# Kernel tuning notes

Measured on AMD Instinct MI355X. Metric: run time of the kernel, lower is better.

The kernel has to match this reference:

```python
import jax, jax.numpy as jnp
import numpy as np

EPS = 1e-5
THRESHOLD = 0.2987


def conv3x3(x, w, stride=1):
    # x: [N,C,H,W], w: [O,I,3,3]
    return jax.lax.conv_general_dilated(
        x, w, window_strides=(stride, stride), padding=((1, 1), (1, 1)),
        dimension_numbers=("NCHW", "OIHW", "NCHW"))


def batchnorm_train(x, gamma, beta):
    # training-mode BN: batch statistics over (N,H,W), biased variance
    mean = jnp.mean(x, axis=(0, 2, 3), keepdims=True)
    var = jnp.var(x, axis=(0, 2, 3), keepdims=True)
    xhat = (x - mean) * jax.lax.rsqrt(var + EPS)
    return xhat * gamma[None, :, None, None] + beta[None, :, None, None]


def setup_inputs() -> dict:
    key = jax.random.key(0)
    k = jax.random.split(key, 7)
    N, C, H, W = 64, 128, 64, 64
    x = jax.random.normal(k[0], (N, C, H, W), dtype=jnp.float32)
    w1 = jax.random.normal(k[1], (C, C, 3, 3), dtype=jnp.float32) * (1.0 / np.sqrt(C * 9))
    gamma1 = jnp.ones((C,), dtype=jnp.float32)
    beta1 = jnp.zeros((C,), dtype=jnp.float32)
    w2 = jax.random.normal(k[2], (C, C, 3, 3), dtype=jnp.float32) * (1.0 / np.sqrt(C * 9))
    gamma2 = jnp.ones((C,), dtype=jnp.float32)
    beta2 = jnp.zeros((C,), dtype=jnp.float32)
    return {"x": x, "w1": w1, "gamma1": gamma1, "beta1": beta1,
            "w2": w2, "gamma2": gamma2, "beta2": beta2}


def reference(x, w1, gamma1, beta1, w2, gamma2, beta2):
    shortcut = x  # stride=1, no down_sample
    out = conv3x3(x, w1, stride=1)
    out = batchnorm_train(out, gamma1, beta1)
    out = jax.nn.relu(out)
    # per-(batch,channel) mean over H,W; zero channels whose mean < threshold
    channel_means = jnp.mean(out, axis=(2, 3))               # [N, C]
    mask = (channel_means >= THRESHOLD).astype(out.dtype)     # [N, C]
    out = out * mask[:, :, None, None]
    out = conv3x3(out, w2, stride=1)
    out = batchnorm_train(out, gamma2, beta2)
    out = out + shortcut
    out = jax.nn.relu(out)
    return out
```

## Files before the change

### kernel.cpp

```cpp
#include <hip/hip_runtime.h>

typedef short short8 __attribute__((ext_vector_type(8)));
typedef short short4v __attribute__((ext_vector_type(4)));
typedef float f32x4 __attribute__((ext_vector_type(4)));
typedef unsigned int u32;

#define EPSF 1e-5f
#define THRF 0.2987f

constexpr int N_ = 64, C_ = 128;
constexpr int PLANE = 4096;
constexpr size_t TENSOR = (size_t)N_ * C_ * PLANE;
constexpr int NHW = N_ * PLANE;
constexpr int PUNITS = 66 * 66 * 8;

__device__ __forceinline__ unsigned short f2bf(float f) {
    unsigned u = __float_as_uint(f);
    u += 0x7fffu + ((u >> 16) & 1u);
    return (unsigned short)(u >> 16);
}
__device__ __forceinline__ float bf2f(unsigned short h) {
    return __uint_as_float((unsigned)h << 16);
}
__device__ __forceinline__ void gld16(const unsigned short* g, unsigned short* l) {
    __builtin_amdgcn_global_load_lds(
        (const __attribute__((address_space(1))) u32*)g,
        (__attribute__((address_space(3))) u32*)l, 16, 0, 0);
}

__global__ __launch_bounds__(256) void prep_w_k(const float* __restrict__ w1,
                                                const float* __restrict__ w2,
                                                unsigned short* __restrict__ Wt1,
                                                unsigned short* __restrict__ Wt2) {
    int idx = blockIdx.x * 256 + threadIdx.x;
    const int sel = idx >= 147456;
    const float* src = sel ? w2 : w1;
    unsigned short* dst = sel ? Wt2 : Wt1;
    const int r = idx - sel * 147456;
    const int tap = r >> 14;
    const int rem = r & 16383;
    const int co = rem >> 7, ci = rem & 127;
    const int half = ci >> 6, csh = (ci >> 5) & 1;
    const int s = half * 18 + tap * 2 + csh;
    dst[(size_t)s * 4096 + co * 32 + (ci & 31)] = f2bf(src[(co * 128 + ci) * 9 + tap]);
}

__global__ __launch_bounds__(256) void zero_border_k(unsigned short* __restrict__ io) {
    int idx = blockIdx.x * 256 + threadIdx.x;
    if (idx >= 266240) return;
    const int plane = idx / 2080;
    const int t = idx - plane * 2080;
    int sp;
    if (t < 528) sp = t >> 3;
    else if (t < 1056) sp = 65 * 66 + ((t - 528) >> 3);
    else if (t < 1568) sp = (((t - 1056) >> 3) + 1) * 66;
    else sp = (((t - 1568) >> 3) + 1) * 66 + 65;
    const size_t off = ((size_t)plane * PUNITS + sp * 8 + (t & 7)) * 8;
    *(short8*)&io[off] = (short8){0, 0, 0, 0, 0, 0, 0, 0};
}

__global__ __launch_bounds__(256) void to_nhwc_k(const float* __restrict__ src,
                                                 unsigned short* __restrict__ dst) {
    __shared__ __align__(16) unsigned short tl[64 * 40];
    const int b = blockIdx.x;
    const int c0 = (b & 3) * 32;
    const int h  = (b >> 2) & 63;
    const int n  = b >> 8;
    const int t  = threadIdx.x;
    for (int i = t; i < 512; i += 256) {
        const int cl = i >> 4;
        const int c  = c0 + cl;
        const int w4 = (i & 15) * 4;
        float4 v = *(const float4*)&src[(size_t)(n * 128 + c) * 4096 + h * 64 + w4];
        tl[(w4 + 0) * 40 + cl] = f2bf(v.x);
        tl[(w4 + 1) * 40 + cl] = f2bf(v.y);
        tl[(w4 + 2) * 40 + cl] = f2bf(v.z);
        tl[(w4 + 3) * 40 + cl] = f2bf(v.w);
    }
    __syncthreads();
    const int w = t >> 2, cs = t & 3;
    short8 v = *(const short8*)&tl[w * 40 + cs * 8];
    const int c = c0 + cs * 8;
    const int half = c >> 6, cig = (c >> 3) & 7;
    const int colp = w + 1, rowp = h + 1;
    const size_t off = ((size_t)(half * 64 + n) * PUNITS
                        + (size_t)(rowp * 66 + colp) * 8 + (cig ^ (colp & 7))) * 8;
    *(short8*)&dst[off] = v;
}

template <int STAGE>
__global__ __launch_bounds__(256, 3) void conv_mfma_k(
    const unsigned short* __restrict__ inT, const unsigned short* __restrict__ Wt,
    const float* __restrict__ msA, const float* __restrict__ mhA,
    unsigned short* __restrict__ outB, float* __restrict__ part) {
    __shared__ __align__(16) unsigned short sIn[2112 * 8];
    __shared__ float fS[256], fQ[256];

    const int b  = (blockIdx.x & 7) * 256 + (blockIdx.x >> 3);
    const int h0 = (b & 31) * 2;
    const int n  = b >> 5;
    const int tid  = threadIdx.x;
    const int lane = tid & 63;
    const int wid  = tid >> 6;
    const int co_base = (wid >> 1) * 64;
    const int px_base = (wid & 1) * 64;
    const int lr = lane & 15;
    const int lg = lane >> 4;

    f32x4 acc[4][4];
#pragma unroll
    for (int i = 0; i < 4; ++i)
#pragma unroll
        for (int j = 0; j < 4; ++j) acc[i][j] = (f32x4){0.f, 0.f, 0.f, 0.f};

    const int nc = n * 128;
    const unsigned short* wlane = Wt + (size_t)(co_base + lr) * 32 + lg * 8;

    int ldsQ[4][2][3];
#pragma unroll
    for (int j = 0; j < 4; ++j) {
        const int px = px_base + j * 16 + lr;
        const int r = px >> 6, c = px & 63;
#pragma unroll
        for (int csh = 0; csh < 2; ++csh)
#pragma unroll
            for (int dc = 0; dc < 3; ++dc) {
                const int cig = csh * 4 + lg;
                ldsQ[j][csh][dc] = (r * 66 + c + dc) * 128 + (cig ^ ((c + dc) & 7)) * 16;
            }
    }

    auto stage_in = [&](int half) {
        const unsigned short* src =
            inT + ((size_t)(half * 64 + n) * PUNITS + (size_t)h0 * 66 * 8) * 8;
        if (STAGE == 1) {
            for (int c = wid; c < 33; c += 4)
                gld16(src + (c * 64 + lane) * 8, &sIn[c * 512]);
        } else {
            const int ncb = nc + half * 64;
            for (int i = tid; i < 2112; i += 256) {
                const int sp = i >> 3, ul = i & 7;
                const int rq = sp / 66;
                const int colp = sp - rq * 66;
                const int rp = h0 + rq;
                short8 v = {0, 0, 0, 0, 0, 0, 0, 0};
                if (rp != 0 && rp != 65 && colp != 0 && colp != 65) {
                    v = *(const short8*)&src[i * 8];
                    const int cig = ul ^ (colp & 7);
                    const int cb = ncb + cig * 8;
                    const float4 m0 = *(const float4*)&msA[cb];
                    const float4 m1 = *(const float4*)&msA[cb + 4];
                    const float4 a0 = *(const float4*)&mhA[cb];
                    const float4 a1 = *(const float4*)&mhA[cb + 4];
                    short8 w;
                    w[0] = (short)f2bf(fmaxf(fmaf(bf2f((unsigned short)v[0]), m0.x, a0.x), 0.f));
                    w[1] = (short)f2bf(fmaxf(fmaf(bf2f((unsigned short)v[1]), m0.y, a0.y), 0.f));
                    w[2] = (short)f2bf(fmaxf(fmaf(bf2f((unsigned short)v[2]), m0.z, a0.z), 0.f));
                    w[3] = (short)f2bf(fmaxf(fmaf(bf2f((unsigned short)v[3]), m0.w, a0.w), 0.f));
                    w[4] = (short)f2bf(fmaxf(fmaf(bf2f((unsigned short)v[4]), m1.x, a1.x), 0.f));
                    w[5] = (short)f2bf(fmaxf(fmaf(bf2f((unsigned short)v[5]), m1.y, a1.y), 0.f));
                    w[6] = (short)f2bf(fmaxf(fmaf(bf2f((unsigned short)v[6]), m1.z, a1.z), 0.f));
                    w[7] = (short)f2bf(fmaxf(fmaf(bf2f((unsigned short)v[7]), m1.w, a1.w), 0.f));
                    v = w;
                }
                *(short8*)&sIn[i * 8] = v;
            }
        }
    };

    auto ldw2 = [&](short8* dst, const unsigned short* p) {
#pragma unroll
        for (int i = 0; i < 4; ++i)
            dst[i] = *(const short8*)&p[i * 512];
    };
    auto ldb = [&](short8* bfv, int dr, int dc, int csh) {
#pragma unroll
        for (int j = 0; j < 4; ++j)
            bfv[j] = *(const short8*)((const char*)sIn + ldsQ[j][csh][dc] + dr * 8448);
    };
    auto mm = [&](short8* af, short8* bfv) {
        __builtin_amdgcn_s_setprio(1);
#pragma unroll
        for (int i = 0; i < 4; ++i)
#pragma unroll
            for (int j = 0; j < 4; ++j)
                acc[i][j] = __builtin_amdgcn_mfma_f32_16x16x32_bf16(af[i], bfv[j],
                                                                    acc[i][j], 0, 0, 0);
        __builtin_amdgcn_s_setprio(0);
    };

    short8 afA[4], afB[4], bfv[4];
    const unsigned short* wpA = wlane;
    const unsigned short* wpB = wlane + 4096;

    stage_in(0);
    ldw2(afA, wpA);
    ldw2(afB, wpB);
    __syncthreads();

#pragma unroll
    for (int half = 0; half < 2; ++half) {
#pragma unroll
        for (int it = 0; it < 9; ++it) {
            const int dr = it / 3, dc = it - dr * 3;
            ldb(bfv, dr, dc, 0);
            mm(afA, bfv);
            if (it < 8) { wpA += 8192; ldw2(afA, wpA); }
            ldb(bfv, dr, dc, 1);
            mm(afB, bfv);
            if (it < 8) { wpB += 8192; ldw2(afB, wpB); }
        }
        if (half == 0) {
            wpA += 8192; ldw2(afA, wpA);
            wpB += 8192; ldw2(afB, wpB);
            __syncthreads();
            stage_in(1);
            __syncthreads();
        }
    }

#pragma unroll
    for (int i = 0; i < 4; ++i)
#pragma unroll
        for (int q = 0; q < 4; ++q) {
            float v = acc[i][0][q] + acc[i][1][q] + acc[i][2][q] + acc[i][3][q];
            float w = acc[i][0][q] * acc[i][0][q] + acc[i][1][q] * acc[i][1][q]
                    + acc[i][2][q] * acc[i][2][q] + acc[i][3][q] * acc[i][3][q];
#pragma unroll
            for (int m = 1; m < 16; m <<= 1) {
                v += __shfl_xor(v, m);
                w += __shfl_xor(w, m);
            }
            if (lr == 0) {
                const int colocal = i * 16 + lg * 4 + q;
                fS[wid * 64 + colocal] = v;
                fQ[wid * 64 + colocal] = w;
            }
        }
    __syncthreads();
    if (tid < 128) {
        const int grp = tid >> 6, cl = tid & 63;
        part[(size_t)b * 256 + tid]       = fS[(grp * 2) * 64 + cl] + fS[(grp * 2 + 1) * 64 + cl];
        part[(size_t)b * 256 + 128 + tid] = fQ[(grp * 2) * 64 + cl] + fQ[(grp * 2 + 1) * 64 + cl];
    }

    if (STAGE == 1) {
        const int h = h0 + (px_base >> 6);
        const int rowp = h + 1;
        const size_t plane = (size_t)((co_base >> 6) * 64 + n) * PUNITS * 8;
        const int pg = lg >> 1;
#pragma unroll
        for (int j = 0; j < 4; ++j) {
            const int w = j * 16 + lr;
            const int colp = w + 1;
            const size_t spoff = plane + (size_t)(rowp * 66 + colp) * 8 * 8;
#pragma unroll
            for (int i = 0; i < 4; ++i) {
                u32 p0 = ((u32)f2bf(acc[i][j][1]) << 16) | f2bf(acc[i][j][0]);
                u32 p1 = ((u32)f2bf(acc[i][j][3]) << 16) | f2bf(acc[i][j][2]);
                const u32 q0 = __shfl_xor(p0, 16);
                const u32 q1 = __shfl_xor(p1, 16);
                if ((lg & 1) == 0) {
                    const int cig = (i * 2 + pg) & 7;
                    u32 st4[4] = {p0, p1, q0, q1};
                    *(short8*)&outB[spoff + (size_t)(cig ^ (colp & 7)) * 8] =
                        *(const short8*)st4;
                }
            }
        }
    } else {
        const size_t outN = (size_t)n * 128 * 4096;
#pragma unroll
        for (int i = 0; i < 4; ++i) {
            const int cob = co_base + i * 16 + lg * 4;
#pragma unroll
            for (int q = 0; q < 4; ++q) {
                unsigned short* op = outB + outN + (size_t)(cob + q) * 4096
                                     + h0 * 64 + px_base + lr;
#pragma unroll
                for (int j = 0; j < 4; ++j) op[j * 16] = f2bf(acc[i][j][q]);
            }
        }
    }
}

__global__ __launch_bounds__(256) void bn_finalize_k(const float* __restrict__ part,
                                                     const float* __restrict__ gamma,
                                                     const float* __restrict__ beta,
                                                     float* __restrict__ st) {
    const int c = blockIdx.x;
    float s = 0.f, q = 0.f;
    for (int b = threadIdx.x; b < 2048; b += 256) {
        s += part[(size_t)b * 256 + c];
        q += part[(size_t)b * 256 + 128 + c];
    }
    __shared__ float rs[256], rq[256];
    rs[threadIdx.x] = s; rq[threadIdx.x] = q;
    __syncthreads();
    for (int o = 128; o > 0; o >>= 1) {
        if (threadIdx.x < o) {
            rs[threadIdx.x] += rs[threadIdx.x + o];
            rq[threadIdx.x] += rq[threadIdx.x + o];
        }
        __syncthreads();
    }
    if (threadIdx.x == 0) {
        const float inv  = 1.f / (float)NHW;
        const float mean = rs[0] * inv;
        const float var  = rq[0] * inv - mean * mean;
        const float sc   = gamma[c] * rsqrtf(var + EPSF);
        st[c]       = sc;
        st[C_ + c]  = fmaf(-mean, sc, beta[c]);
    }
}

__global__ __launch_bounds__(256) void maskpart_k(const unsigned short* __restrict__ y1,
                                                  const float* __restrict__ st,
                                                  float* __restrict__ msA,
                                                  float* __restrict__ mhA) {
    const int n = blockIdx.x >> 1, half = blockIdx.x & 1;
    const int t = threadIdx.x;
    const int colg = t & 63;
    const int p = t >> 6;
    const int colp = 1 + colg;
    float scv[2][8], shv[2][8], a[2][8];
#pragma unroll
    for (int k = 0; k < 2; ++k)
#pragma unroll
        for (int e = 0; e < 8; ++e) {
            const int c = half * 64 + (2 * p + k) * 8 + e;
            scv[k][e] = st[c];
            shv[k][e] = st[128 + c];
            a[k][e] = 0.f;
        }
    const size_t plane = (size_t)(half * 64 + n) * PUNITS * 8;
    for (int rowp = 1; rowp <= 64; ++rowp) {
        const int sp = rowp * 66 + colp;
#pragma unroll
        for (int k = 0; k < 2; ++k) {
            const int cig = 2 * p + k;
            short8 v = *(const short8*)&y1[plane + ((size_t)sp * 8 + (cig ^ (colp & 7))) * 8];
#pragma unroll
            for (int e = 0; e < 8; ++e)
                a[k][e] += fmaxf(fmaf(bf2f((unsigned short)v[e]), scv[k][e], shv[k][e]), 0.f);
        }
    }
    __shared__ float lds[256][16];
#pragma unroll
    for (int k = 0; k < 2; ++k)
#pragma unroll
        for (int e = 0; e < 8; ++e) lds[t][k * 8 + e] = a[k][e];
    __syncthreads();
    if (t < 64) {
        const int cig = t >> 3, e = t & 7, p2 = cig >> 1, k2 = cig & 1;
        float s = 0.f;
        for (int cg = 0; cg < 64; ++cg) s += lds[p2 * 64 + cg][k2 * 8 + e];
        const int c = half * 64 + t;
        const float m = (s * (1.f / 4096.f) >= THRF) ? 1.f : 0.f;
        msA[n * 128 + c] = st[c] * m;
        mhA[n * 128 + c] = st[128 + c] * m;
    }
}

__global__ __launch_bounds__(256) void final_k(const unsigned short* __restrict__ y3,
                                               const float* __restrict__ x,
                                               const float* __restrict__ st,
                                               float* __restrict__ out) {
    const size_t total8 = TENSOR / 8;
    for (size_t g = (size_t)blockIdx.x * 256 + threadIdx.x; g < total8;
         g += (size_t)gridDim.x * 256) {
        const int c = (int)((g >> 9) & (C_ - 1));
        const float sc = st[c], sh = st[C_ + c];
        short8 yv = *(const short8*)&y3[g * 8];
        float4 a0 = ((const float4*)x)[g * 2];
        float4 a1 = ((const float4*)x)[g * 2 + 1];
        float4 o0, o1;
        o0.x = fmaxf(fmaf(bf2f((unsigned short)yv[0]), sc, sh) + a0.x, 0.f);
        o0.y = fmaxf(fmaf(bf2f((unsigned short)yv[1]), sc, sh) + a0.y, 0.f);
        o0.z = fmaxf(fmaf(bf2f((unsigned short)yv[2]), sc, sh) + a0.z, 0.f);
        o0.w = fmaxf(fmaf(bf2f((unsigned short)yv[3]), sc, sh) + a0.w, 0.f);
        o1.x = fmaxf(fmaf(bf2f((unsigned short)yv[4]), sc, sh) + a1.x, 0.f);
        o1.y = fmaxf(fmaf(bf2f((unsigned short)yv[5]), sc, sh) + a1.y, 0.f);
        o1.z = fmaxf(fmaf(bf2f((unsigned short)yv[6]), sc, sh) + a1.z, 0.f);
        o1.w = fmaxf(fmaf(bf2f((unsigned short)yv[7]), sc, sh) + a1.w, 0.f);
        ((float4*)out)[g * 2]     = o0;
        ((float4*)out)[g * 2 + 1] = o1;
    }
}

extern "C" void kernel_launch(void* const* d_in, const int* in_sizes, int n_in,
                              void* d_out, int out_size, void* d_ws, size_t ws_size,
                              hipStream_t stream) {
    const float* x  = (const float*)d_in[0];
    const float* w1 = (const float*)d_in[1];
    const float* g1 = (const float*)d_in[2];
    const float* b1 = (const float*)d_in[3];
    const float* w2 = (const float*)d_in[4];
    const float* g2 = (const float*)d_in[5];
    const float* b2 = (const float*)d_in[6];
    float* out = (float*)d_out;

    unsigned short* y1 = (unsigned short*)d_out;

    char* wsb = (char*)d_ws;
    unsigned short* io  = (unsigned short*)wsb;
    unsigned short* y3b = (unsigned short*)wsb;
    unsigned short* Wt1 = (unsigned short*)(wsb + (size_t)71368704);
    unsigned short* Wt2 = Wt1 + 147456;
    float* part = (float*)(wsb + (size_t)71368704 + 589824);
    float* st1  = part + 2048 * 256;
    float* st2  = st1 + 256;
    float* msA  = st2 + 256;
    float* mhA  = msA + 64 * 128;

    prep_w_k<<<1152, 256, 0, stream>>>(w1, w2, Wt1, Wt2);
    zero_border_k<<<1040, 256, 0, stream>>>(io);
    to_nhwc_k<<<16384, 256, 0, stream>>>(x, io);
    conv_mfma_k<1><<<2048, 256, 0, stream>>>(io, Wt1, nullptr, nullptr, y1, part);
    bn_finalize_k<<<128, 256, 0, stream>>>(part, g1, b1, st1);
    maskpart_k<<<128, 256, 0, stream>>>(y1, st1, msA, mhA);
    conv_mfma_k<2><<<2048, 256, 0, stream>>>(y1, Wt2, msA, mhA, y3b, part);
    bn_finalize_k<<<128, 256, 0, stream>>>(part, g2, b2, st2);
    final_k<<<8192, 256, 0, stream>>>(y3b, x, st2, out);
}
```

Baseline: 328.6 us.

## Prefetch second channel half into registers during MFMA loop; split mask reduction

```diff
diff --git a/kernel.cpp b/kernel.cpp
--- a/kernel.cpp
+++ b/kernel.cpp
@@ -130,14 +130,13 @@
             }
     }
 
-    auto stage_in = [&](int half) {
-        const unsigned short* src =
-            inT + ((size_t)(half * 64 + n) * PUNITS + (size_t)h0 * 66 * 8) * 8;
+    auto stage_h0 = [&]() {
+        const unsigned short* src = inT + ((size_t)n * PUNITS + (size_t)h0 * 66 * 8) * 8;
         if (STAGE == 1) {
             for (int c = wid; c < 33; c += 4)
                 gld16(src + (c * 64 + lane) * 8, &sIn[c * 512]);
         } else {
-            const int ncb = nc + half * 64;
+            const int ncb = nc;
             for (int i = tid; i < 2112; i += 256) {
                 const int sp = i >> 3, ul = i & 7;
                 const int rq = sp / 66;
@@ -189,14 +188,24 @@
         __builtin_amdgcn_s_setprio(0);
     };
 
-    short8 afA[4], afB[4], bfv[4];
+    short8 afA[4], afB[4], bfv[4], pre[9];
     const unsigned short* wpA = wlane;
     const unsigned short* wpB = wlane + 4096;
 
-    stage_in(0);
+    stage_h0();
     ldw2(afA, wpA);
     ldw2(afB, wpB);
     __syncthreads();
+
+    {
+        const unsigned short* src1 =
+            inT + ((size_t)(64 + n) * PUNITS + (size_t)h0 * 66 * 8) * 8;
+#pragma unroll
+        for (int k = 0; k < 8; ++k)
+            pre[k] = *(const short8*)&src1[(size_t)(tid + k * 256) * 8];
+        pre[8] = (tid < 64) ? *(const short8*)&src1[(size_t)(2048 + tid) * 8]
+                            : (short8){0, 0, 0, 0, 0, 0, 0, 0};
+    }
 
 #pragma unroll
     for (int half = 0; half < 2; ++half) {
@@ -214,7 +223,44 @@
             wpA += 8192; ldw2(afA, wpA);
             wpB += 8192; ldw2(afB, wpB);
             __syncthreads();
-            stage_in(1);
+            if (STAGE == 1) {
+#pragma unroll
+                for (int k = 0; k < 9; ++k) {
+                    const int idx = tid + k * 256;
+                    if (k < 8 || tid < 64)
+                        *(short8*)&sIn[(size_t)idx * 8] = pre[k];
+                }
+            } else {
+                const int ncb = nc + 64;
+#pragma unroll
+                for (int k = 0; k < 9; ++k) {
+                    const int idx = tid + k * 256;
+                    if (k == 8 && tid >= 64) continue;
+                    const int sp = idx >> 3, ul = idx & 7;
+                    const int rq = sp / 66;
+                    const int colp = sp - rq * 66;
+                    const int rp = h0 + rq;
+                    short8 v = {0, 0, 0, 0, 0, 0, 0, 0};
+                    if (rp != 0 && rp != 65 && colp != 0 && colp != 65) {
+                        const short8 pv = pre[k];
+                        const int cig = ul ^ (colp & 7);
+                        const int cb = ncb + cig * 8;
+                        const float4 m0 = *(const float4*)&msA[cb];
+                        const float4 m1 = *(const float4*)&msA[cb + 4];
+                        const float4 a0 = *(const float4*)&mhA[cb];
+                        const float4 a1 = *(const float4*)&mhA[cb + 4];
+                        v[0] = (short)f2bf(fmaxf(fmaf(bf2f((unsigned short)pv[0]), m0.x, a0.x), 0.f));
+                        v[1] = (short)f2bf(fmaxf(fmaf(bf2f((unsigned short)pv[1]), m0.y, a0.y), 0.f));
+                        v[2] = (short)f2bf(fmaxf(fmaf(bf2f((unsigned short)pv[2]), m0.z, a0.z), 0.f));
+                        v[3] = (short)f2bf(fmaxf(fmaf(bf2f((unsigned short)pv[3]), m0.w, a0.w), 0.f));
+                        v[4] = (short)f2bf(fmaxf(fmaf(bf2f((unsigned short)pv[4]), m1.x, a1.x), 0.f));
+                        v[5] = (short)f2bf(fmaxf(fmaf(bf2f((unsigned short)pv[5]), m1.y, a1.y), 0.f));
+                        v[6] = (short)f2bf(fmaxf(fmaf(bf2f((unsigned short)pv[6]), m1.z, a1.z), 0.f));
+                        v[7] = (short)f2bf(fmaxf(fmaf(bf2f((unsigned short)pv[7]), m1.w, a1.w), 0.f));
+                    }
+                    *(short8*)&sIn[(size_t)idx * 8] = v;
+                }
+            }
             __syncthreads();
         }
     }
@@ -316,9 +362,9 @@
 
 __global__ __launch_bounds__(256) void maskpart_k(const unsigned short* __restrict__ y1,
                                                   const float* __restrict__ st,
-                                                  float* __restrict__ msA,
-                                                  float* __restrict__ mhA) {
-    const int n = blockIdx.x >> 1, half = blockIdx.x & 1;
+                                                  float* __restrict__ qsum) {
+    const int blk = blockIdx.x;
+    const int n = blk >> 3, half = (blk >> 2) & 1, rq = blk & 3;
     const int t = threadIdx.x;
     const int colg = t & 63;
     const int p = t >> 6;
@@ -334,7 +380,7 @@
             a[k][e] = 0.f;
         }
     const size_t plane = (size_t)(half * 64 + n) * PUNITS * 8;
-    for (int rowp = 1; rowp <= 64; ++rowp) {
+    for (int rowp = rq * 16 + 1; rowp <= rq * 16 + 16; ++rowp) {
         const int sp = rowp * 66 + colp;
 #pragma unroll
         for (int k = 0; k < 2; ++k) {
@@ -355,11 +401,22 @@
         const int cig = t >> 3, e = t & 7, p2 = cig >> 1, k2 = cig & 1;
         float s = 0.f;
         for (int cg = 0; cg < 64; ++cg) s += lds[p2 * 64 + cg][k2 * 8 + e];
-        const int c = half * 64 + t;
-        const float m = (s * (1.f / 4096.f) >= THRF) ? 1.f : 0.f;
-        msA[n * 128 + c] = st[c] * m;
-        mhA[n * 128 + c] = st[128 + c] * m;
-    }
+        qsum[(size_t)blk * 64 + t] = s;
+    }
+}
+
+__global__ void maskfin_k(const float* __restrict__ qsum, const float* __restrict__ st,
+                          float* __restrict__ msA, float* __restrict__ mhA) {
+    const int n = blockIdx.x, c = threadIdx.x;
+    if (c >= 128) return;
+    const int half = c >> 6, cl = c & 63;
+    float s = 0.f;
+#pragma unroll
+    for (int rq = 0; rq < 4; ++rq)
+        s += qsum[(size_t)(n * 8 + half * 4 + rq) * 64 + cl];
+    const float m = (s * (1.f / 4096.f) >= THRF) ? 1.f : 0.f;
+    msA[n * 128 + c] = st[c] * m;
+    mhA[n * 128 + c] = st[128 + c] * m;
 }
 
 __global__ __launch_bounds__(256) void final_k(const unsigned short* __restrict__ y3,
@@ -412,13 +469,15 @@
     float* st2  = st1 + 256;
     float* msA  = st2 + 256;
     float* mhA  = msA + 64 * 128;
+    float* qsum = mhA + 64 * 128;
 
     prep_w_k<<<1152, 256, 0, stream>>>(w1, w2, Wt1, Wt2);
     zero_border_k<<<1040, 256, 0, stream>>>(io);
     to_nhwc_k<<<16384, 256, 0, stream>>>(x, io);
     conv_mfma_k<1><<<2048, 256, 0, stream>>>(io, Wt1, nullptr, nullptr, y1, part);
     bn_finalize_k<<<128, 256, 0, stream>>>(part, g1, b1, st1);
-    maskpart_k<<<128, 256, 0, stream>>>(y1, st1, msA, mhA);
+    maskpart_k<<<512, 256, 0, stream>>>(y1, st1, qsum);
+    maskfin_k<<<64, 128, 0, stream>>>(qsum, st1, msA, mhA);
     conv_mfma_k<2><<<2048, 256, 0, stream>>>(y1, Wt2, msA, mhA, y3b, part);
     bn_finalize_k<<<128, 256, 0, stream>>>(part, g2, b2, st2);
     final_k<<<8192, 256, 0, stream>>>(y3b, x, st2, out);
```

New measurement: 326.1 us. Within noise of the previous version (-0.8%).
